# Kernel optimization log

Measured on AMD Instinct MI355X. Metric: run time of the kernel, lower is better.

## Reference

```python
import jax, jax.numpy as jnp
import numpy as np

T, N, E = 4, 50000, 400000
F0, F1, F2 = 128, 128, 64


def _xavier(k, shape):
    a = float(np.sqrt(6.0 / (shape[0] + shape[1])))
    return jax.random.uniform(k, shape, jnp.float32, -a, a)


def setup_inputs() -> dict:
    key = jax.random.key(0)
    ks = jax.random.split(key, 32)
    inp = {
        'node_embs': jax.random.normal(ks[0], (T, N, F0), jnp.float32),
        'mask': jnp.zeros((T, N, 1), jnp.float32),
        'edge_src': jax.random.randint(ks[1], (T, E), 0, N, jnp.int32),
        'edge_dst': jax.random.randint(ks[2], (T, E), 0, N, jnp.int32),
        'edge_weight': jax.random.uniform(ks[3], (T, E), jnp.float32),
        'gcn_w0': _xavier(ks[4], (F0, F1)),
        'gcn_w1': _xavier(ks[5], (F1, F2)),
    }
    i = 6
    for (pre, rows, cols) in (('l0', F0, F1), ('l1', F1, F2)):
        for g in ('u', 'r', 'h'):
            inp[pre + '_W' + g] = _xavier(ks[i], (rows, rows)); i += 1
            inp[pre + '_U' + g] = _xavier(ks[i], (rows, rows)); i += 1
            inp[pre + '_B' + g] = jnp.zeros((rows, cols), jnp.float32)
        inp[pre + '_scorer'] = _xavier(ks[i], (rows, 1)); i += 1
    return inp


def _topk_embed(X, m, scorer, k):
    # scores: [N,1] = X @ scorer / ||scorer|| + mask
    scores = X @ scorer / jnp.linalg.norm(scorer) + m
    vals, idx = jax.lax.top_k(scores[:, 0], k)          # [k]
    return (X[idx] * jnp.tanh(vals)[:, None]).T         # [rows, k]


def _grcu(Q0, params, node_seq, mask_seq, src, dst, ew, k, n_nodes):
    Wu, Uu, Bu, Wr, Ur, Br, Wh, Uh, Bh, scorer = params

    def step(Q, xs):
        X, m, s, d, w = xs
        z = _topk_embed(X, m, scorer, k)                 # [rows, cols]
        upd = jax.nn.sigmoid(Wu @ z + Uu @ Q + Bu)
        rst = jax.nn.sigmoid(Wr @ z + Ur @ Q + Br)
        hcap = jnp.tanh(Wh @ z + Uh @ (rst * Q) + Bh)
        Qn = (1.0 - upd) * Q + upd * hcap                # evolved GCN weight
        XW = X @ Qn                                      # [N, cols]
        msg = XW[s] * w[:, None]                         # gather + scale
        out = jax.nn.relu(jax.ops.segment_sum(msg, d, num_segments=n_nodes))
        return Qn, out

    _, outs = jax.lax.scan(step, Q0, (node_seq, mask_seq, src, dst, ew))
    return outs  # [T, N, cols]


def reference(node_embs, mask, edge_src, edge_dst, edge_weight, gcn_w0, gcn_w1,
              l0_Wu, l0_Uu, l0_Bu, l0_Wr, l0_Ur, l0_Br, l0_Wh, l0_Uh, l0_Bh, l0_scorer,
              l1_Wu, l1_Uu, l1_Bu, l1_Wr, l1_Ur, l1_Br, l1_Wh, l1_Uh, l1_Bh, l1_scorer):
    p0 = (l0_Wu, l0_Uu, l0_Bu, l0_Wr, l0_Ur, l0_Br, l0_Wh, l0_Uh, l0_Bh, l0_scorer)
    p1 = (l1_Wu, l1_Uu, l1_Bu, l1_Wr, l1_Ur, l1_Br, l1_Wh, l1_Uh, l1_Bh, l1_scorer)
    n = node_embs.shape[1]
    h1 = _grcu(gcn_w0, p0, node_embs, mask, edge_src, edge_dst, edge_weight, gcn_w0.shape[1], n)
    h2 = _grcu(gcn_w1, p1, h1, mask, edge_src, edge_dst, edge_weight, gcn_w1.shape[1], n)
    return h2  # [T, N, F2]
```

## Files before the change

### kernel.cpp

```cpp
#include <hip/hip_runtime.h>
#include <math.h>

#define T_STEPS 4
#define NNODES 50000
#define NEDGES 400000
#define FIN 128
#define NBINS 8192
#define BINSHIFT 19
#define EQCAP 4096
#define DSHARD 6250

__device__ __forceinline__ float sigmoidf_(float x) { return 1.0f / (1.0f + __expf(-x)); }

__device__ __forceinline__ unsigned int key_of(float s) {
    unsigned int u = __float_as_uint(s);
    return (u & 0x80000000u) ? ~u : (u | 0x80000000u);
}

__device__ __forceinline__ unsigned short f2bf(float f) {
    unsigned int u = __float_as_uint(f);
    unsigned int r = (u + 0x7FFFu + ((u >> 16) & 1u)) >> 16;
    return (unsigned short)r;
}
__device__ __forceinline__ float bf2f(unsigned short h) {
    return __uint_as_float(((unsigned int)h) << 16);
}

typedef float f4v __attribute__((ext_vector_type(4)));
__device__ __forceinline__ void nt_store4(float* p, float4 v) {
    f4v w; w.x = v.x; w.y = v.y; w.z = v.z; w.w = v.w;
    __builtin_nontemporal_store(w, (f4v*)p);
}

__global__ void norm_kernel(const float* __restrict__ s0, const float* __restrict__ s1,
                            float* __restrict__ norms) {
    __shared__ float red[128];
    int tid = threadIdx.x;
    float a = s0[tid];
    red[tid] = a * a;
    __syncthreads();
    for (int off = 64; off > 0; off >>= 1) { if (tid < off) red[tid] += red[tid + off]; __syncthreads(); }
    if (tid == 0) norms[0] = sqrtf(red[0]);
    __syncthreads();
    float b = s1[tid];
    red[tid] = b * b;
    __syncthreads();
    for (int off = 64; off > 0; off >>= 1) { if (tid < off) red[tid] += red[tid + off]; __syncthreads(); }
    if (tid == 0) norms[1] = sqrtf(red[0]);
}

__global__ void scores_hist4_kernel(const float* __restrict__ node_embs, const float* __restrict__ scorer,
                                    const float* __restrict__ norms,
                                    const float* __restrict__ mask, float* __restrict__ scores4,
                                    int* __restrict__ ghist4, int N) {
    __shared__ float sc[FIN];
    if (threadIdx.x < FIN) sc[threadIdx.x] = scorer[threadIdx.x];
    __syncthreads();
    int t = blockIdx.y;
    int n = blockIdx.x * blockDim.x + threadIdx.x;
    if (n >= N) return;
    const float4* xr = (const float4*)(node_embs + ((size_t)t * N + n) * FIN);
    float acc = 0.f;
#pragma unroll 8
    for (int k4 = 0; k4 < FIN / 4; k4++) {
        float4 v = xr[k4];
        acc += v.x * sc[k4 * 4] + v.y * sc[k4 * 4 + 1] + v.z * sc[k4 * 4 + 2] + v.w * sc[k4 * 4 + 3];
    }
    float s = acc / norms[0] + mask[(size_t)t * N + n];
    scores4[(size_t)t * N + n] = s;
    atomicAdd(&ghist4[t * NBINS + (key_of(s) >> BINSHIFT)], 1);
}

__global__ void __launch_bounds__(256)
topk_collect_kernel(const float* __restrict__ scores_b, const int* __restrict__ ghist_b,
                    int* __restrict__ cnts_b, int* __restrict__ gt_idx_b, float* __restrict__ gt_val_b,
                    int* __restrict__ eq_idx_b, float* __restrict__ eq_val_b, int N, int K) {
    __shared__ int h[NBINS];
    __shared__ int part[256];
    __shared__ int s_bin;
    int tid = threadIdx.x;
    int task = blockIdx.y;
    const int* gh = ghist_b + (size_t)task * NBINS;
    for (int i = tid; i < NBINS; i += 256) h[i] = gh[i];
    __syncthreads();
    int s = 0;
#pragma unroll
    for (int i = 0; i < NBINS / 256; i++) s += h[tid * (NBINS / 256) + i];
    part[tid] = s;
    __syncthreads();
    for (int off = 1; off < 256; off <<= 1) {
        int v = (tid + off < 256) ? part[tid + off] : 0;
        __syncthreads();
        part[tid] += v;
        __syncthreads();
    }
    {
        int run = (tid == 255) ? 0 : part[tid + 1];
        const int CH = NBINS / 256;
        for (int b = tid * CH + CH - 1; b >= tid * CH; b--) {
            int Sb = run + h[b];
            if (Sb >= K && run < K) s_bin = b;
            run = Sb;
        }
    }
    __syncthreads();
    int bin = s_bin;
    const float* scores = scores_b + (size_t)task * N;
    int* cg = cnts_b + task * 2;
    for (int n = blockIdx.x * 256 + tid; n < N; n += gridDim.x * 256) {
        float sc = scores[n];
        unsigned int key = key_of(sc);
        int kb = (int)(key >> BINSHIFT);
        if (kb > bin) {
            int p = atomicAdd(&cg[0], 1);
            gt_idx_b[task * 128 + p] = n; gt_val_b[task * 128 + p] = sc;
        } else if (kb == bin) {
            int p = atomicAdd(&cg[1], 1);
            if (p < EQCAP) { eq_idx_b[task * EQCAP + p] = n; eq_val_b[task * EQCAP + p] = sc; }
        }
    }
}

template <int K>
__global__ void __launch_bounds__(1024)
topk_finish_kernel(int* __restrict__ ghist_b, int* __restrict__ cnts_b,
                   const int* __restrict__ gt_idx_b, const float* __restrict__ gt_val_b,
                   const int* __restrict__ eq_idx_b, const float* __restrict__ eq_val_b,
                   const float* __restrict__ X_b, float* __restrict__ z_b, int N) {
    __shared__ int sidx[K];
    __shared__ float sval[K];
    __shared__ unsigned int ek[EQCAP];
    __shared__ int ei[EQCAP];
    __shared__ int out_idx[K];
    __shared__ float out_tanh[K];
    int tid = threadIdx.x;
    int task = blockIdx.x;
    int* cg = cnts_b + task * 2;
    int g = cg[0];
    int m = min(cg[1], EQCAP);
    int need = K - g;
    const int* gt_idx = gt_idx_b + task * 128;
    const float* gt_val = gt_val_b + task * 128;
    const int* eq_idx = eq_idx_b + task * EQCAP;
    const float* eq_val = eq_val_b + task * EQCAP;
    const float* X = X_b + (size_t)task * N * FIN;
    float* z = z_b + (size_t)task * FIN * K;

    for (int i = tid; i < g; i += 1024) { sidx[i] = gt_idx[i]; sval[i] = gt_val[i]; }
    for (int i = tid; i < m; i += 1024) { ek[i] = key_of(eq_val[i]); ei[i] = eq_idx[i]; }
    __syncthreads();
    for (int i = tid; i < m; i += 1024) {
        int myi = ei[i];
        unsigned int myk = ek[i];
        int rank = 0;
        for (int j = 0; j < m; j++)
            rank += (ek[j] > myk) || (ek[j] == myk && ei[j] < myi);
        if (rank < need) { sidx[g + rank] = myi; sval[g + rank] = eq_val[i]; }
    }
    __syncthreads();
    if (tid < K) {
        float v = sval[tid];
        int id = sidx[tid];
        unsigned int myk = key_of(v);
        int rank = 0;
        for (int j = 0; j < K; j++) {
            unsigned int kj = key_of(sval[j]);
            rank += (kj > myk) || (kj == myk && sidx[j] < id);
        }
        out_idx[rank] = id;
        out_tanh[rank] = tanhf(v);
    }
    int* gh = ghist_b + (size_t)task * NBINS;
    for (int i = tid; i < NBINS; i += 1024) gh[i] = 0;
    if (tid == 0) { cg[0] = 0; cg[1] = 0; }
    __syncthreads();
    for (int i = tid; i < K * FIN; i += 1024) {
        int j = i >> 7;
        int r = i & 127;
        z[r * K + j] = X[(size_t)out_idx[j] * FIN + r] * out_tanh[j];
    }
}

template <int COLS>
__global__ void __launch_bounds__(256)
gru_multi_kernel(const float* __restrict__ Qinit, const float* __restrict__ z_all,
                 const float* __restrict__ Wu, const float* __restrict__ Uu, const float* __restrict__ Bu,
                 const float* __restrict__ Wr, const float* __restrict__ Ur, const float* __restrict__ Br,
                 const float* __restrict__ Wh, const float* __restrict__ Uh, const float* __restrict__ Bh,
                 float* __restrict__ Qn_all) {
    __shared__ float zc[128][8];
    __shared__ float qc[128][8];
    __shared__ float rq[128][8];
    __shared__ float ul[128][8];
    int tid = threadIdx.x;
    int c0 = blockIdx.x * 8;
    for (int i = tid; i < 1024; i += 256) {
        int r = i >> 3, c = i & 7;
        qc[r][c] = Qinit[r * COLS + c0 + c];
    }
    for (int t = 0; t < T_STEPS; t++) {
        __syncthreads();
        const float* z = z_all + (size_t)t * 128 * COLS;
        for (int i = tid; i < 1024; i += 256) {
            int r = i >> 3, c = i & 7;
            zc[r][c] = z[r * COLS + c0 + c];
        }
        __syncthreads();
#pragma unroll
        for (int e = 0; e < 4; e++) {
            int idx = tid + 256 * e;
            int r = idx >> 3, c = idx & 7;
            float au = Bu[r * COLS + c0 + c], ar = Br[r * COLS + c0 + c];
            for (int k = 0; k < 128; k++) {
                float zz = zc[k][c], qq = qc[k][c];
                au += Wu[r * 128 + k] * zz + Uu[r * 128 + k] * qq;
                ar += Wr[r * 128 + k] * zz + Ur[r * 128 + k] * qq;
            }
            ul[r][c] = sigmoidf_(au);
            rq[r][c] = sigmoidf_(ar) * qc[r][c];
        }
        __syncthreads();
        float* Qn = Qn_all + (size_t)t * 128 * COLS;
#pragma unroll
        for (int e = 0; e < 4; e++) {
            int idx = tid + 256 * e;
            int r = idx >> 3, c = idx & 7;
            float s = Bh[r * COLS + c0 + c];
            for (int k = 0; k < 128; k++) {
                s += Wh[r * 128 + k] * zc[k][c] + Uh[r * 128 + k] * rq[k][c];
            }
            float h = tanhf(s);
            float u = ul[r][c];
            float qn = (1.f - u) * qc[r][c] + u * h;
            Qn[r * COLS + c0 + c] = qn;
            qc[r][c] = qn;
        }
    }
}

template <bool BF16>
__global__ void __launch_bounds__(256)
xw_kernel(const float* __restrict__ X_b, const float* __restrict__ Qn_all,
          void* __restrict__ outp, int N, int ostride) {
    constexpr int SW = 64;
    constexpr int TPR = SW / 4;
    constexpr int RPG = 256 / TPR;
    constexpr int RPB = RPG * 4;
    int t = blockIdx.y;
    int coff = blockIdx.z * SW;
    const float* X = X_b + (size_t)t * N * FIN;
    const float* Qn = Qn_all + (size_t)t * 128 * ostride;
    __shared__ float4 qs[128 * TPR];
    for (int i = threadIdx.x; i < 128 * TPR; i += 256) {
        int r = i / TPR, c4 = i % TPR;
        qs[i] = *(const float4*)(Qn + (size_t)r * ostride + coff + c4 * 4);
    }
    __syncthreads();
    int lane_c = threadIdx.x % TPR;
    int rloc = threadIdx.x / TPR;
    int base = blockIdx.x * RPB;
    int rows[4];
    float4 acc[4];
#pragma unroll
    for (int j = 0; j < 4; j++) {
        rows[j] = base + rloc + j * RPG;
        acc[j] = make_float4(0.f, 0.f, 0.f, 0.f);
    }
    int nc[4];
#pragma unroll
    for (int j = 0; j < 4; j++) nc[j] = min(rows[j], N - 1);

    for (int k4 = 0; k4 < 32; k4++) {
        float4 q0 = qs[(k4 * 4 + 0) * TPR + lane_c];
        float4 q1 = qs[(k4 * 4 + 1) * TPR + lane_c];
        float4 q2 = qs[(k4 * 4 + 2) * TPR + lane_c];
        float4 q3 = qs[(k4 * 4 + 3) * TPR + lane_c];
#pragma unroll
        for (int j = 0; j < 4; j++) {
            float4 xv = ((const float4*)(X + (size_t)nc[j] * FIN))[k4];
            acc[j].x += xv.x * q0.x + xv.y * q1.x + xv.z * q2.x + xv.w * q3.x;
            acc[j].y += xv.x * q0.y + xv.y * q1.y + xv.z * q2.y + xv.w * q3.y;
            acc[j].z += xv.x * q0.z + xv.y * q1.z + xv.z * q2.z + xv.w * q3.z;
            acc[j].w += xv.x * q0.w + xv.y * q1.w + xv.z * q2.w + xv.w * q3.w;
        }
    }
#pragma unroll
    for (int j = 0; j < 4; j++) {
        if (rows[j] < N) {
            if (BF16) {
                ushort4 o;
                o.x = f2bf(acc[j].x); o.y = f2bf(acc[j].y);
                o.z = f2bf(acc[j].z); o.w = f2bf(acc[j].w);
                ((ushort4*)((unsigned short*)outp + ((size_t)t * N + rows[j]) * ostride + coff))[lane_c] = o;
            } else {
                ((float4*)((float*)outp + ((size_t)t * N + rows[j]) * ostride + coff))[lane_c] = acc[j];
            }
        }
    }
}

__global__ void hist4_kernel(const int* __restrict__ dst, int* __restrict__ hist4, int E) {
    int e = blockIdx.x * blockDim.x + threadIdx.x;
    if (e >= E) return;
    int t = blockIdx.y;
    atomicAdd(&hist4[t * NNODES + dst[(size_t)t * E + e]], 1);
}

__global__ void __launch_bounds__(256)
scanA_kernel(const int* __restrict__ hist, int* __restrict__ incl, int* __restrict__ bsum, int M) {
    __shared__ int sh[256];
    int gid = blockIdx.x * 256 + threadIdx.x;
    int v = (gid < M) ? hist[gid] : 0;
    sh[threadIdx.x] = v;
    __syncthreads();
    for (int off = 1; off < 256; off <<= 1) {
        int u = (threadIdx.x >= off) ? sh[threadIdx.x - off] : 0;
        __syncthreads();
        sh[threadIdx.x] += u;
        __syncthreads();
    }
    if (gid < M) incl[gid] = sh[threadIdx.x];
    if (threadIdx.x == 255) bsum[blockIdx.x] = sh[255];
}

__global__ void __launch_bounds__(1024)
scanB_kernel(int* __restrict__ bsum, int nb) {
    __shared__ int sh[1024];
    int tid = threadIdx.x;
    int v = (tid < nb) ? bsum[tid] : 0;
    sh[tid] = v;
    __syncthreads();
    for (int off = 1; off < 1024; off <<= 1) {
        int u = (tid >= off) ? sh[tid - off] : 0;
        __syncthreads();
        sh[tid] += u;
        __syncthreads();
    }
    if (tid < nb) bsum[tid] = (tid == 0) ? 0 : sh[tid - 1];
}

__global__ void __launch_bounds__(256)
scanC_kernel(const int* __restrict__ hist, const int* __restrict__ incl,
             const int* __restrict__ bsum, int* __restrict__ row_ptr,
             int* __restrict__ cursor, int M) {
    int gid = blockIdx.x * 256 + threadIdx.x;
    if (gid < M) {
        int inc = incl[gid] + bsum[gid / 256];
        int ex = inc - hist[gid];
        row_ptr[gid] = ex;
        cursor[gid] = ex;
        if (gid == M - 1) row_ptr[M] = inc;
    }
}

__global__ void bucket4_kernel(const int* __restrict__ src, const int* __restrict__ dst,
                               const float* __restrict__ w, int* __restrict__ cursor,
                               int2* __restrict__ sedge, int E) {
    int bx = blockIdx.x;
    int shard = bx & 7;
    int e = (bx >> 3) * 256 + threadIdx.x;
    if (e >= E) return;
    int t = blockIdx.y;
    size_t ge = (size_t)t * E + e;
    int d = dst[ge];
    if (d / DSHARD != shard) return;
    int pos = atomicAdd(&cursor[t * NNODES + d], 1);
    int2 pk;
    pk.x = src[ge];
    pk.y = __float_as_int(w[ge]);
    sedge[pos] = pk;
}

template <int SW, bool SCORE>
__global__ void __launch_bounds__(256)
agg_slice_kernel(const float* __restrict__ XW_b, const int* __restrict__ row_ptr4,
                 const int2* __restrict__ sedge,
                 float* __restrict__ out_b, int N, int P,
                 const float* __restrict__ scorer, const float* __restrict__ norms,
                 const float* __restrict__ mask_b, float* __restrict__ scores_b,
                 int* __restrict__ ghist_b, float* __restrict__ scoreacc) {
    constexpr int TPN = SW / 4;
    constexpr int NPB = 256 / TPN;
    constexpr int NPASS = FIN / SW;
    int lin = blockIdx.x;
    int xcd = lin & 7;
    int slot = lin >> 3;
    int t = xcd >> 1;
    int db = slot * 2 + (xcd & 1);
    int dstBlocks = (N + NPB - 1) / NPB;
    if (db >= dstBlocks) return;
    int node = db * NPB + threadIdx.x / TPN;
    if (node >= N) return;
    int lane = threadIdx.x % TPN;
    const int* rp = row_ptr4 + (size_t)t * N;
    int beg = rp[node], end = rp[node + 1];
    const float* XW = XW_b + (size_t)t * N * FIN + P * SW;
    float4 a0 = make_float4(0.f, 0.f, 0.f, 0.f);
    float4 a1 = a0, a2 = a0, a3 = a0;
    int i = beg;
    for (; i + 4 <= end; i += 4) {
        int2 p0 = sedge[i], p1 = sedge[i + 1], p2 = sedge[i + 2], p3 = sedge[i + 3];
        float4 v0 = ((const float4*)(XW + (size_t)p0.x * FIN))[lane];
        float4 v1 = ((const float4*)(XW + (size_t)p1.x * FIN))[lane];
        float4 v2 = ((const float4*)(XW + (size_t)p2.x * FIN))[lane];
        float4 v3 = ((const float4*)(XW + (size_t)p3.x * FIN))[lane];
        float w0 = __int_as_float(p0.y), w1 = __int_as_float(p1.y);
        float w2 = __int_as_float(p2.y), w3 = __int_as_float(p3.y);
        a0.x += v0.x * w0; a0.y += v0.y * w0; a0.z += v0.z * w0; a0.w += v0.w * w0;
        a1.x += v1.x * w1; a1.y += v1.y * w1; a1.z += v1.z * w1; a1.w += v1.w * w1;
        a2.x += v2.x * w2; a2.y += v2.y * w2; a2.z += v2.z * w2; a2.w += v2.w * w2;
        a3.x += v3.x * w3; a3.y += v3.y * w3; a3.z += v3.z * w3; a3.w += v3.w * w3;
    }
    for (; i < end; i++) {
        int2 pk = sedge[i];
        float wt = __int_as_float(pk.y);
        float4 v = ((const float4*)(XW + (size_t)pk.x * FIN))[lane];
        a0.x += v.x * wt; a0.y += v.y * wt; a0.z += v.z * wt; a0.w += v.w * wt;
    }
    float4 acc;
    acc.x = (a0.x + a1.x) + (a2.x + a3.x);
    acc.y = (a0.y + a1.y) + (a2.y + a3.y);
    acc.z = (a0.z + a1.z) + (a2.z + a3.z);
    acc.w = (a0.w + a1.w) + (a2.w + a3.w);
    acc.x = fmaxf(acc.x, 0.f); acc.y = fmaxf(acc.y, 0.f);
    acc.z = fmaxf(acc.z, 0.f); acc.w = fmaxf(acc.w, 0.f);
    nt_store4(out_b + ((size_t)t * N + node) * FIN + P * SW + lane * 4, acc);
    if (SCORE) {
        float4 sc4 = ((const float4*)(scorer + P * SW))[lane];
        float partial = acc.x * sc4.x + acc.y * sc4.y + acc.z * sc4.z + acc.w * sc4.w;
#pragma unroll
        for (int off = TPN / 2; off > 0; off >>= 1) partial += __shfl_xor(partial, off, TPN);
        if (lane == 0) {
            float* sa = scoreacc + (size_t)t * N + node;
            float tot = (P == 0 ? 0.f : *sa) + partial;
            if (P == NPASS - 1) {
                float s = tot / norms[1] + mask_b[(size_t)t * N + node];
                scores_b[(size_t)t * N + node] = s;
                atomicAdd(&ghist_b[t * NBINS + (key_of(s) >> BINSHIFT)], 1);
            } else {
                *sa = tot;
            }
        }
    }
}

template <int COLS>
__global__ void __launch_bounds__(256)
agg_kernel(const unsigned short* __restrict__ XWb, const int* __restrict__ row_ptr4,
           const int2* __restrict__ sedge,
           float* __restrict__ out_b, int N) {
    constexpr int TPN = COLS / 4;
    constexpr int NPB = 256 / TPN;
    int lin = blockIdx.x;
    int xcd = lin & 7;
    int slot = lin >> 3;
    int t = xcd >> 1;
    int db = slot * 2 + (xcd & 1);
    int dstBlocks = (N + NPB - 1) / NPB;
    if (db >= dstBlocks) return;
    int node = db * NPB + threadIdx.x / TPN;
    if (node >= N) return;
    int lane = threadIdx.x % TPN;
    const int* rp = row_ptr4 + (size_t)t * N;
    int beg = rp[node], end = rp[node + 1];
    const unsigned short* XW = XWb + (size_t)t * N * COLS;
    float4 a0 = make_float4(0.f, 0.f, 0.f, 0.f);
    float4 a1 = a0, a2 = a0, a3 = a0;
    int i = beg;
    for (; i + 4 <= end; i += 4) {
        int2 p0 = sedge[i], p1 = sedge[i + 1], p2 = sedge[i + 2], p3 = sedge[i + 3];
        ushort4 v0 = ((const ushort4*)(XW + (size_t)p0.x * COLS))[lane];
        ushort4 v1 = ((const ushort4*)(XW + (size_t)p1.x * COLS))[lane];
        ushort4 v2 = ((const ushort4*)(XW + (size_t)p2.x * COLS))[lane];
        ushort4 v3 = ((const ushort4*)(XW + (size_t)p3.x * COLS))[lane];
        float w0 = __int_as_float(p0.y), w1 = __int_as_float(p1.y);
        float w2 = __int_as_float(p2.y), w3 = __int_as_float(p3.y);
        a0.x += bf2f(v0.x) * w0; a0.y += bf2f(v0.y) * w0; a0.z += bf2f(v0.z) * w0; a0.w += bf2f(v0.w) * w0;
        a1.x += bf2f(v1.x) * w1; a1.y += bf2f(v1.y) * w1; a1.z += bf2f(v1.z) * w1; a1.w += bf2f(v1.w) * w1;
        a2.x += bf2f(v2.x) * w2; a2.y += bf2f(v2.y) * w2; a2.z += bf2f(v2.z) * w2; a2.w += bf2f(v2.w) * w2;
        a3.x += bf2f(v3.x) * w3; a3.y += bf2f(v3.y) * w3; a3.z += bf2f(v3.z) * w3; a3.w += bf2f(v3.w) * w3;
    }
    for (; i < end; i++) {
        int2 pk = sedge[i];
        float wt = __int_as_float(pk.y);
        ushort4 v = ((const ushort4*)(XW + (size_t)pk.x * COLS))[lane];
        a0.x += bf2f(v.x) * wt; a0.y += bf2f(v.y) * wt;
        a0.z += bf2f(v.z) * wt; a0.w += bf2f(v.w) * wt;
    }
    float4 acc;
    acc.x = (a0.x + a1.x) + (a2.x + a3.x);
    acc.y = (a0.y + a1.y) + (a2.y + a3.y);
    acc.z = (a0.z + a1.z) + (a2.z + a3.z);
    acc.w = (a0.w + a1.w) + (a2.w + a3.w);
    acc.x = fmaxf(acc.x, 0.f); acc.y = fmaxf(acc.y, 0.f);
    acc.z = fmaxf(acc.z, 0.f); acc.w = fmaxf(acc.w, 0.f);
    nt_store4(out_b + ((size_t)t * N + node) * COLS + lane * 4, acc);
}

extern "C" void kernel_launch(void* const* d_in, const int* in_sizes, int n_in,
                              void* d_out, int out_size, void* d_ws, size_t ws_size,
                              hipStream_t stream) {
    const float* node_embs   = (const float*)d_in[0];
    const float* mask        = (const float*)d_in[1];
    const int*   edge_src    = (const int*)d_in[2];
    const int*   edge_dst    = (const int*)d_in[3];
    const float* edge_weight = (const float*)d_in[4];
    const float* gcn_w0      = (const float*)d_in[5];
    const float* gcn_w1      = (const float*)d_in[6];
    const float* l0p[10];
    const float* l1p[10];
    for (int i = 0; i < 10; i++) l0p[i] = (const float*)d_in[7 + i];
    for (int i = 0; i < 10; i++) l1p[i] = (const float*)d_in[17 + i];

    char* ws = (char*)d_ws;
    size_t off = 0;
    auto alloc = [&](size_t bytes) -> void* {
        void* p = ws + off;
        off += (bytes + 255) / 256 * 256;
        return p;
    };
    float* XW0buf = (float*)alloc((size_t)4 * NNODES * 128 * 4);
    float* h1buf  = (float*)alloc((size_t)4 * NNODES * 128 * 4);
    unsigned short* XW1buf = (unsigned short*)alloc((size_t)4 * NNODES * 64 * 2);
    float* scores4= (float*)alloc((size_t)4 * NNODES * 4);
    float* scores1= (float*)alloc((size_t)4 * NNODES * 4);
    float* scoreacc=(float*)alloc((size_t)4 * NNODES * 4);
    float* z0buf  = (float*)alloc((size_t)4 * 128 * 128 * 4);
    float* z1buf  = (float*)alloc((size_t)4 * 128 * 64 * 4);
    float* Q0n    = (float*)alloc((size_t)4 * 128 * 128 * 4);
    float* Q1n    = (float*)alloc((size_t)4 * 128 * 64 * 4);
    float* norms  = (float*)alloc(64);
    int* hist4    = (int*)alloc(((size_t)4 * NNODES + 8 * NBINS + 64) * 4);
    int* ghist0   = hist4 + 4 * NNODES;
    int* ghist1   = ghist0 + 4 * NBINS;
    int* cnts     = ghist1 + 4 * NBINS;
    int* incl4    = (int*)alloc((size_t)4 * NNODES * 4);
    int* bsumb    = (int*)alloc(1024 * 4);
    int* rowp4    = (int*)alloc(((size_t)4 * NNODES + 1) * 4);
    int* cursor4  = (int*)alloc((size_t)4 * NNODES * 4);
    int2* sedge4  = (int2*)alloc((size_t)4 * NEDGES * 8);
    int*   gt_idx = (int*)alloc((size_t)4 * 128 * 4);
    float* gt_val = (float*)alloc((size_t)4 * 128 * 4);
    int*   eq_idx = (int*)alloc((size_t)4 * EQCAP * 4);
    float* eq_val = (float*)alloc((size_t)4 * EQCAP * 4);

    hipMemsetAsync(hist4, 0, ((size_t)4 * NNODES + 8 * NBINS + 64) * 4, stream);
    norm_kernel<<<1, 128, 0, stream>>>(l0p[9], l1p[9], norms);

    const int M4 = 4 * NNODES;
    const int NB4 = (M4 + 255) / 256;
    const int NB = (NNODES + 255) / 256;
    const int EB = (NEDGES + 255) / 256;

    hist4_kernel<<<dim3(EB, 4), 256, 0, stream>>>(edge_dst, hist4, NEDGES);
    scanA_kernel<<<NB4, 256, 0, stream>>>(hist4, incl4, bsumb, M4);
    scanB_kernel<<<1, 1024, 0, stream>>>(bsumb, NB4);
    scanC_kernel<<<NB4, 256, 0, stream>>>(hist4, incl4, bsumb, rowp4, cursor4, M4);
    bucket4_kernel<<<dim3(EB * 8, 4), 256, 0, stream>>>(edge_src, edge_dst, edge_weight, cursor4, sedge4, NEDGES);

    scores_hist4_kernel<<<dim3(NB, 4), 256, 0, stream>>>(node_embs, l0p[9], norms, mask, scores4, ghist0, NNODES);
    topk_collect_kernel<<<dim3(NB, 4), 256, 0, stream>>>(scores4, ghist0, cnts, gt_idx, gt_val, eq_idx, eq_val, NNODES, 128);
    topk_finish_kernel<128><<<4, 1024, 0, stream>>>(ghist0, cnts, gt_idx, gt_val, eq_idx, eq_val, node_embs, z0buf, NNODES);

    gru_multi_kernel<128><<<16, 256, 0, stream>>>(gcn_w0, z0buf,
        l0p[0], l0p[1], l0p[2], l0p[3], l0p[4], l0p[5], l0p[6], l0p[7], l0p[8], Q0n);
    {
        const int RB = (NNODES + 63) / 64;
        xw_kernel<false><<<dim3(RB, 4, 2), 256, 0, stream>>>(node_embs, Q0n, XW0buf, NNODES, 128);
    }
    {
        const int dstBlocksS = (NNODES + 31) / 32;
        const int gridS = ((dstBlocksS + 1) / 2) * 8;
        for (int P = 0; P < 4; P++) {
            agg_slice_kernel<32, true><<<gridS, 256, 0, stream>>>(XW0buf, rowp4, sedge4, h1buf, NNODES, P,
                l1p[9], norms, mask, scores1, ghist1, scoreacc);
        }
    }

    topk_collect_kernel<<<dim3(NB, 4), 256, 0, stream>>>(scores1, ghist1, cnts, gt_idx, gt_val, eq_idx, eq_val, NNODES, 64);
    topk_finish_kernel<64><<<4, 1024, 0, stream>>>(ghist1, cnts, gt_idx, gt_val, eq_idx, eq_val, h1buf, z1buf, NNODES);
    gru_multi_kernel<64><<<8, 256, 0, stream>>>(gcn_w1, z1buf,
        l1p[0], l1p[1], l1p[2], l1p[3], l1p[4], l1p[5], l1p[6], l1p[7], l1p[8], Q1n);
    {
        const int RB = (NNODES + 63) / 64;
        xw_kernel<true><<<dim3(RB, 4, 1), 256, 0, stream>>>(h1buf, Q1n, XW1buf, NNODES, 64);
    }
    {
        const int dstBlocks1 = (NNODES + 15) / 16;
        const int grid1 = ((dstBlocks1 + 1) / 2) * 8;
        agg_kernel<64><<<grid1, 256, 0, stream>>>(XW1buf, rowp4, sedge4, (float*)d_out, NNODES);
    }
}
```

Before: 1.150 ms.

## Parallelize GRU weight evolution per column with gate-split threads

The GRU kernel now assigns one block per output column instead of eight columns per block, raising the grid from 16/8 blocks to 128/64. Within a block the 256 threads split into two halves that compute the update and reset gates in parallel, with float4 row-wise loads of the weight matrices against shared vectors. This aims to shorten a latency-bound serial kernel by using far more CUs. The cost is that each block rereads the full weight matrices, so total weight traffic grows, though it should mostly be served from cache.

```diff
diff --git a/kernel.cpp b/kernel.cpp
--- a/kernel.cpp
+++ b/kernel.cpp
@@ -188,52 +188,57 @@
                  const float* __restrict__ Wr, const float* __restrict__ Ur, const float* __restrict__ Br,
                  const float* __restrict__ Wh, const float* __restrict__ Uh, const float* __restrict__ Bh,
                  float* __restrict__ Qn_all) {
-    __shared__ float zc[128][8];
-    __shared__ float qc[128][8];
-    __shared__ float rq[128][8];
-    __shared__ float ul[128][8];
+    __shared__ float zc[128];
+    __shared__ float qc[128];
+    __shared__ float rq[128];
+    __shared__ float ul[128];
     int tid = threadIdx.x;
-    int c0 = blockIdx.x * 8;
-    for (int i = tid; i < 1024; i += 256) {
-        int r = i >> 3, c = i & 7;
-        qc[r][c] = Qinit[r * COLS + c0 + c];
-    }
+    int c = blockIdx.x;
+    int r = tid & 127;
+    int gate = tid >> 7;
+    if (tid < 128) qc[tid] = Qinit[tid * COLS + c];
     for (int t = 0; t < T_STEPS; t++) {
         __syncthreads();
         const float* z = z_all + (size_t)t * 128 * COLS;
-        for (int i = tid; i < 1024; i += 256) {
-            int r = i >> 3, c = i & 7;
-            zc[r][c] = z[r * COLS + c0 + c];
-        }
-        __syncthreads();
-#pragma unroll
-        for (int e = 0; e < 4; e++) {
-            int idx = tid + 256 * e;
-            int r = idx >> 3, c = idx & 7;
-            float au = Bu[r * COLS + c0 + c], ar = Br[r * COLS + c0 + c];
-            for (int k = 0; k < 128; k++) {
-                float zz = zc[k][c], qq = qc[k][c];
-                au += Wu[r * 128 + k] * zz + Uu[r * 128 + k] * qq;
-                ar += Wr[r * 128 + k] * zz + Ur[r * 128 + k] * qq;
+        if (tid < 128) zc[tid] = z[tid * COLS + c];
+        __syncthreads();
+        {
+            const float* W = gate ? Wr : Wu;
+            const float* U = gate ? Ur : Uu;
+            const float* B = gate ? Br : Bu;
+            const float4* W4 = (const float4*)(W + r * 128);
+            const float4* U4 = (const float4*)(U + r * 128);
+            const float4* z4 = (const float4*)zc;
+            const float4* q4 = (const float4*)qc;
+            float aw = 0.f, au = 0.f;
+#pragma unroll 8
+            for (int k4 = 0; k4 < 32; k4++) {
+                float4 w = W4[k4], u = U4[k4], zz = z4[k4], qq = q4[k4];
+                aw += w.x * zz.x + w.y * zz.y + w.z * zz.z + w.w * zz.w;
+                au += u.x * qq.x + u.y * qq.y + u.z * qq.z + u.w * qq.w;
             }
-            ul[r][c] = sigmoidf_(au);
-            rq[r][c] = sigmoidf_(ar) * qc[r][c];
-        }
-        __syncthreads();
-        float* Qn = Qn_all + (size_t)t * 128 * COLS;
-#pragma unroll
-        for (int e = 0; e < 4; e++) {
-            int idx = tid + 256 * e;
-            int r = idx >> 3, c = idx & 7;
-            float s = Bh[r * COLS + c0 + c];
-            for (int k = 0; k < 128; k++) {
-                s += Wh[r * 128 + k] * zc[k][c] + Uh[r * 128 + k] * rq[k][c];
+            float a = sigmoidf_(B[r * COLS + c] + aw + au);
+            if (gate == 0) ul[r] = a;
+            else rq[r] = a * qc[r];
+        }
+        __syncthreads();
+        if (tid < 128) {
+            const float4* W4 = (const float4*)(Wh + r * 128);
+            const float4* U4 = (const float4*)(Uh + r * 128);
+            const float4* z4 = (const float4*)zc;
+            const float4* rq4 = (const float4*)rq;
+            float aw = 0.f, au = 0.f;
+#pragma unroll 8
+            for (int k4 = 0; k4 < 32; k4++) {
+                float4 w = W4[k4], u = U4[k4], zz = z4[k4], qq = rq4[k4];
+                aw += w.x * zz.x + w.y * zz.y + w.z * zz.z + w.w * zz.w;
+                au += u.x * qq.x + u.y * qq.y + u.z * qq.z + u.w * qq.w;
             }
-            float h = tanhf(s);
-            float u = ul[r][c];
-            float qn = (1.f - u) * qc[r][c] + u * h;
-            Qn[r * COLS + c0 + c] = qn;
-            qc[r][c] = qn;
+            float h = tanhf(Bh[r * COLS + c] + aw + au);
+            float u = ul[r];
+            float qn = (1.f - u) * qc[r] + u * h;
+            Qn_all[(size_t)t * 128 * COLS + r * COLS + c] = qn;
+            qc[r] = qn;
         }
     }
 }
@@ -562,7 +567,7 @@
     topk_collect_kernel<<<dim3(NB, 4), 256, 0, stream>>>(scores4, ghist0, cnts, gt_idx, gt_val, eq_idx, eq_val, NNODES, 128);
     topk_finish_kernel<128><<<4, 1024, 0, stream>>>(ghist0, cnts, gt_idx, gt_val, eq_idx, eq_val, node_embs, z0buf, NNODES);
 
-    gru_multi_kernel<128><<<16, 256, 0, stream>>>(gcn_w0, z0buf,
+    gru_multi_kernel<128><<<128, 256, 0, stream>>>(gcn_w0, z0buf,
         l0p[0], l0p[1], l0p[2], l0p[3], l0p[4], l0p[5], l0p[6], l0p[7], l0p[8], Q0n);
     {
         const int RB = (NNODES + 63) / 64;
@@ -579,7 +584,7 @@
 
     topk_collect_kernel<<<dim3(NB, 4), 256, 0, stream>>>(scores1, ghist1, cnts, gt_idx, gt_val, eq_idx, eq_val, NNODES, 64);
     topk_finish_kernel<64><<<4, 1024, 0, stream>>>(ghist1, cnts, gt_idx, gt_val, eq_idx, eq_val, h1buf, z1buf, NNODES);
-    gru_multi_kernel<64><<<8, 256, 0, stream>>>(gcn_w1, z1buf,
+    gru_multi_kernel<64><<<64, 256, 0, stream>>>(gcn_w1, z1buf,
         l1p[0], l1p[1], l1p[2], l1p[3], l1p[4], l1p[5], l1p[6], l1p[7], l1p[8], Q1n);
     {
         const int RB = (NNODES + 63) / 64;
```

Measured after the change: 1.005 ms. -12.7%, faster.
